# Kernel optimization log

Hardware: AMD Instinct MI355X
Metric: run time of the kernel (lower is better)

## Reference

```python
import jax, jax.numpy as jnp
import numpy as np

B, T, D, H, L = 2048, 100, 51, 128, 3  # batch, window, vars, latent, layers


def _lstm_cell(x, h, c, Wih, Whh, b):
    # PyTorch gate order: i, f, g, o. b = b_ih + b_hh (mathematically identical).
    g = x @ Wih.T + h @ Whh.T + b
    i, f, gg, o = jnp.split(g, 4, axis=-1)
    i = jax.nn.sigmoid(i)
    f = jax.nn.sigmoid(f)
    gg = jnp.tanh(gg)
    o = jax.nn.sigmoid(o)
    c_new = f * c + i * gg
    h_new = o * jnp.tanh(c_new)
    return h_new, c_new


def _run_layer(xs, Wih, Whh, b):
    # xs: [T, B, in]; returns full h sequence and final (h, c)
    bsz = xs.shape[1]
    h0 = jnp.zeros((bsz, H), xs.dtype)
    c0 = jnp.zeros((bsz, H), xs.dtype)

    def step(carry, x):
        h, c = carry
        h, c = _lstm_cell(x, h, c, Wih, Whh, b)
        return (h, c), h

    (hT, cT), hs = jax.lax.scan(step, (h0, c0), xs)
    return hs, hT, cT


def setup_inputs() -> dict:
    key = jax.random.key(0)
    ks = iter(jax.random.split(key, 32))
    s = 0.05

    def w(shape):
        return jax.random.normal(next(ks), shape, dtype=jnp.float32) * s

    inp = {"src": jax.random.normal(next(ks), (B, T, D), dtype=jnp.float32)}
    # encoder LSTM params (layer0 input=D, layers1-2 input=H)
    for l in range(L):
        din = D if l == 0 else H
        inp[f"eW{l}"] = w((4 * H, din))
        inp[f"eU{l}"] = w((4 * H, H))
        inp[f"eb{l}"] = w((4 * H,))
    # decoder LSTM params (same input sizes: input_size=input_dim)
    for l in range(L):
        din = D if l == 0 else H
        inp[f"dW{l}"] = w((4 * H, din))
        inp[f"dU{l}"] = w((4 * H, H))
        inp[f"db{l}"] = w((4 * H,))
    inp["fW"] = w((D, H))
    inp["fb"] = w((D,))
    return inp


def reference(src, eW0, eU0, eb0, eW1, eU1, eb1, eW2, eU2, eb2,
              dW0, dU0, db0, dW1, dU1, db1, dW2, dU2, db2, fW, fb):
    bsz, seq, dvar = src.shape
    xs = jnp.transpose(src, (1, 0, 2))  # [T, B, D]

    # ----- encoder: 3 stacked LSTM layers (dropout is identity at eval) -----
    enc = [(eW0, eU0, eb0), (eW1, eU1, eb1), (eW2, eU2, eb2)]
    hs_fin, cs_fin = [], []
    cur = xs
    for (Wih, Whh, b) in enc:
        cur, hT, cT = _run_layer(cur, Wih, Whh, b)
        hs_fin.append(hT)
        cs_fin.append(cT)

    dec = [(dW0, dU0, db0), (dW1, dU1, db1), (dW2, dU2, db2)]
    x0 = jnp.zeros((bsz, dvar), src.dtype)

    def dec_step(carry, _):
        x, (h0, h1, h2), (c0, c1, c2) = carry
        h0, c0 = _lstm_cell(x, h0, c0, *dec[0])
        h1, c1 = _lstm_cell(h0, h1, c1, *dec[1])
        h2, c2 = _lstm_cell(h1, h2, c2, *dec[2])
        pred = h2 @ fW.T + fb  # note: self.relu is defined but never applied
        return (pred, (h0, h1, h2), (c0, c1, c2)), pred

    carry0 = (x0, tuple(hs_fin), tuple(cs_fin))
    _, preds = jax.lax.scan(dec_step, carry0, None, length=seq)  # [T, B, D]

    # cat along time then reverse time axis (inv_idx)
    out = jnp.transpose(preds, (1, 0, 2))[:, ::-1, :]
    return out
```

## Files before the change

kernel.cpp:

```cpp
#include <hip/hip_runtime.h>
#include <stdint.h>

#define Tn 100
#define Dn 51
#define Hn 128
#define G4 512
#define BR 8
#define NWG 256
#define NTH 1024
#define RP 264

typedef unsigned int uint32;
typedef unsigned short u16;
typedef short s16x8 __attribute__((ext_vector_type(8)));
typedef float f32x4v __attribute__((ext_vector_type(4)));

__device__ __forceinline__ float rcp_(float x){ return __builtin_amdgcn_rcpf(x); }
__device__ __forceinline__ float sigm(float x){ return rcp_(1.f + __expf(-x)); }
__device__ __forceinline__ float tanh_(float x){ return 1.f - 2.f*rcp_(1.f + __expf(2.f*x)); }

__device__ __forceinline__ u16 f2bf(float f){
  uint32 u = __float_as_uint(f);
  return (u16)((u + 0x7fffu + ((u >> 16) & 1u)) >> 16);
}
__device__ __forceinline__ float bf2f(u16 u){ return __uint_as_float(((uint32)u)<<16); }

__device__ __forceinline__ void wr_xh(u16* __restrict__ xhA, int r, int k, float v){
  u16 h = f2bf(v);
  xhA[r*RP + k]     = h;
  xhA[(r+8)*RP + k] = f2bf(v - bf2f(h));
}

struct WP {
  const float* W[6];
  const float* U[6];
  const float* Bb[6];
  const float* fW;
  const float* fb;
};

#define PREP_TOTAL (6*131072 + 6*512 + 8192 + 64)
__global__ void prep_kernel(WP p, u16* __restrict__ wsw, float* __restrict__ bias,
                            float* __restrict__ fwt, float* __restrict__ fbw)
{
  int gid = blockIdx.x*256 + threadIdx.x;
  if (gid >= PREP_TOTAL) return;
  if (gid < 6*131072){
    int l = gid >> 17;
    int e = gid & 131071;
    int n    = e >> 12;
    int s    = (e >> 9) & 7;
    int lane = (e >> 3) & 63;
    int j    = e & 7;
    int k = s*32 + (lane >> 4)*8 + j;
    int c = n*16 + (lane & 15);
    int din = (l % 3 == 0) ? Dn : Hn;
    int K = din + Hn;
    u16 v = 0;
    if (k < K){
      float f = (k < din) ? p.W[l][(size_t)c*din + k] : p.U[l][(size_t)c*Hn + (k - din)];
      v = f2bf(f);
    }
    wsw[gid] = v;
  } else if (gid < 6*131072 + 6*512){
    int i = gid - 6*131072;
    bias[i] = p.Bb[i>>9][i & 511];
  } else if (gid < 6*131072 + 6*512 + 8192){
    int i = gid - (6*131072 + 6*512);
    int k = i >> 6, d = i & 63;
    fwt[i] = (d < Dn) ? p.fW[(size_t)d*Hn + k] : 0.f;
  } else {
    int d = gid - (6*131072 + 6*512 + 8192);
    fbw[d] = (d < Dn) ? p.fb[d] : 0.f;
  }
}

template<int S>
__device__ __forceinline__ void gemm_mfma(const u16* __restrict__ wsl,
                                          const float* __restrict__ bl,
                                          const u16* __restrict__ xhA,
                                          float* __restrict__ gates, int tid)
{
  const int wave = tid >> 6, lane = tid & 63;
  const int mrow = lane & 15, kgrp = lane >> 4;
  const int n0 = wave*2;
  const u16* bp0 = wsl + n0*4096 + lane*8;
  const int aoff = mrow*RP + kgrp*8;
  f32x4v acc0 = {0.f,0.f,0.f,0.f}, acc1 = {0.f,0.f,0.f,0.f};
  #pragma unroll 2
  for (int s=0; s<S; s++){
    s16x8 a  = *(const s16x8*)(xhA + aoff + s*32);
    s16x8 b0 = *(const s16x8*)(bp0 + s*512);
    s16x8 b1 = *(const s16x8*)(bp0 + 4096 + s*512);
    acc0 = __builtin_amdgcn_mfma_f32_16x16x32_bf16(a, b0, acc0, 0, 0, 0);
    acc1 = __builtin_amdgcn_mfma_f32_16x16x32_bf16(a, b1, acc1, 0, 0, 0);
  }
  #pragma unroll
  for (int v=0; v<4; v++){
    float l0 = __shfl_down(acc0[v], 32);
    float l1 = __shfl_down(acc1[v], 32);
    acc0[v] += l0;
    acc1[v] += l1;
  }
  if (kgrp < 2){
    int rb = kgrp*4;
    int c0g = n0*16 + mrow, c1g = c0g + 16;
    float bv0 = bl[c0g], bv1 = bl[c1g];
    #pragma unroll
    for (int v=0; v<4; v++){
      gates[(rb+v)*G4 + c0g] = acc0[v] + bv0;
      gates[(rb+v)*G4 + c1g] = acc1[v] + bv1;
    }
  }
}

__device__ __forceinline__ void activate(const float* __restrict__ gates,
                                         float* __restrict__ h, float* __restrict__ c, int tid)
{
  int r = tid >> 7, j = tid & 127;
  const float* g = gates + r*G4;
  float ig = sigm (g[j]);
  float fg = sigm (g[j + Hn]);
  float gg = tanh_(g[j + 2*Hn]);
  float og = sigm (g[j + 3*Hn]);
  int hi = r*Hn + j;
  float cn = fg*c[hi] + ig*gg;
  c[hi] = cn;
  h[hi] = og*tanh_(cn);
}

__device__ __forceinline__ void build_src(u16* __restrict__ xhA,
                                          const float* __restrict__ src,
                                          long b0, int t, const float* __restrict__ h0, int tid)
{
  int k = tid & 255;
  #pragma unroll
  for (int it=0; it<2; it++){
    int r = (tid >> 8) + it*4;
    if (k < 192){
      float v;
      if (k < Dn) v = src[((size_t)(b0+r)*Tn + t)*Dn + k];
      else if (k < Dn + Hn) v = h0[r*Hn + (k - Dn)];
      else v = 0.f;
      wr_xh(xhA, r, k, v);
    }
  }
}

__device__ __forceinline__ void build_pred(u16* __restrict__ xhA,
                                           const float* __restrict__ pred,
                                           const float* __restrict__ h0, int tid)
{
  int k = tid & 255;
  #pragma unroll
  for (int it=0; it<2; it++){
    int r = (tid >> 8) + it*4;
    if (k < 192){
      float v;
      if (k < Dn) v = pred[r*64 + k];
      else if (k < Dn + Hn) v = h0[r*Hn + (k - Dn)];
      else v = 0.f;
      wr_xh(xhA, r, k, v);
    }
  }
}

__device__ __forceinline__ void build_mid(u16* __restrict__ xhA,
                                          const float* __restrict__ hlow,
                                          const float* __restrict__ hl, int tid)
{
  int k = tid & 255;
  #pragma unroll
  for (int it=0; it<2; it++){
    int r = (tid >> 8) + it*4;
    float v = (k < Hn) ? hlow[r*Hn + k] : hl[r*Hn + (k - Hn)];
    wr_xh(xhA, r, k, v);
  }
}

__device__ __forceinline__ void proj_out(const float* __restrict__ h2, const float* __restrict__ fwt,
                                         const float* __restrict__ fbw, float* __restrict__ pred,
                                         float* __restrict__ out, long b0, int t, int tid)
{
  if (tid < 512){
    int r = tid >> 6, d = tid & 63;
    const float* h = h2 + r*Hn;
    float acc = 0.f;
    #pragma unroll 8
    for (int k=0;k<Hn;k++) acc += h[k] * fwt[k*64 + d];
    if (d < Dn){
      float pv = acc + fbw[d];
      pred[r*64 + d] = pv;
      out[((size_t)(b0+r)*Tn + (Tn-1-t))*Dn + d] = pv;
    }
  }
}

__global__ __launch_bounds__(NTH, 4) void lstm_kernel(
    const float* __restrict__ src, const u16* __restrict__ wsw,
    const float* __restrict__ bias, const float* __restrict__ fwt,
    const float* __restrict__ fbw, float* __restrict__ out)
{
  __shared__ __align__(16) u16   xhA[16*RP];
  __shared__ __align__(16) float gates[BR*G4];
  __shared__ __align__(16) float hS[3*BR*Hn];
  __shared__ __align__(16) float cS[3*BR*Hn];
  __shared__ __align__(16) float pred[BR*64];

  const int tid = threadIdx.x;
  const long b0 = (long)blockIdx.x * BR;

  for (int i=tid; i<16*RP; i+=NTH) xhA[i]=0;
  for (int i=tid; i<3*BR*Hn; i+=NTH){ hS[i]=0.f; cS[i]=0.f; }
  __syncthreads();

  for (int t=0;t<Tn;t++){
    build_src(xhA, src, b0, t, hS, tid);
    __syncthreads();
    gemm_mfma<6>(wsw + 0*131072, bias + 0*G4, xhA, gates, tid);
    __syncthreads();
    activate(gates, hS, cS, tid);
    __syncthreads();

    build_mid(xhA, hS, hS + BR*Hn, tid);
    __syncthreads();
    gemm_mfma<8>(wsw + 1*131072, bias + 1*G4, xhA, gates, tid);
    __syncthreads();
    activate(gates, hS + BR*Hn, cS + BR*Hn, tid);
    __syncthreads();

    build_mid(xhA, hS + BR*Hn, hS + 2*BR*Hn, tid);
    __syncthreads();
    gemm_mfma<8>(wsw + 2*131072, bias + 2*G4, xhA, gates, tid);
    __syncthreads();
    activate(gates, hS + 2*BR*Hn, cS + 2*BR*Hn, tid);
    __syncthreads();
  }

  if (tid < 512) pred[tid] = 0.f;
  __syncthreads();

  for (int t=0;t<Tn;t++){
    build_pred(xhA, pred, hS, tid);
    __syncthreads();
    gemm_mfma<6>(wsw + 3*131072, bias + 3*G4, xhA, gates, tid);
    __syncthreads();
    activate(gates, hS, cS, tid);
    __syncthreads();

    build_mid(xhA, hS, hS + BR*Hn, tid);
    __syncthreads();
    gemm_mfma<8>(wsw + 4*131072, bias + 4*G4, xhA, gates, tid);
    __syncthreads();
    activate(gates, hS + BR*Hn, cS + BR*Hn, tid);
    __syncthreads();

    build_mid(xhA, hS + BR*Hn, hS + 2*BR*Hn, tid);
    __syncthreads();
    gemm_mfma<8>(wsw + 5*131072, bias + 5*G4, xhA, gates, tid);
    __syncthreads();
    activate(gates, hS + 2*BR*Hn, cS + 2*BR*Hn, tid);
    __syncthreads();

    proj_out(hS + 2*BR*Hn, fwt, fbw, pred, out, b0, t, tid);
    __syncthreads();
  }
}

extern "C" void kernel_launch(void* const* d_in, const int* in_sizes, int n_in,
                              void* d_out, int out_size, void* d_ws, size_t ws_size,
                              hipStream_t stream)
{
  (void)in_sizes; (void)n_in; (void)out_size; (void)ws_size;
  const float* src = (const float*)d_in[0];
  WP p;
  for (int l=0;l<3;l++){
    p.W[l]    = (const float*)d_in[1  + 3*l];
    p.U[l]    = (const float*)d_in[2  + 3*l];
    p.Bb[l]   = (const float*)d_in[3  + 3*l];
    p.W[3+l]  = (const float*)d_in[10 + 3*l];
    p.U[3+l]  = (const float*)d_in[11 + 3*l];
    p.Bb[3+l] = (const float*)d_in[12 + 3*l];
  }
  p.fW = (const float*)d_in[19];
  p.fb = (const float*)d_in[20];

  u16*   wsw  = (u16*)d_ws;
  float* bias = (float*)((char*)d_ws + 6*131072*sizeof(u16));
  float* fwt  = bias + 6*512;
  float* fbw  = fwt + 8192;

  prep_kernel<<<(PREP_TOTAL + 255)/256, 256, 0, stream>>>(p, wsw, bias, fwt, fbw);
  lstm_kernel<<<NWG, NTH, 0, stream>>>(src, wsw, bias, fwt, fbw, (float*)d_out);
}
```

Before: 2.054 ms.

## Prefetch next-layer weight fragments into registers and fuse xh building into activation

Weight B-fragments for the next layer's GEMM are loaded into registers while the current GEMM runs, so global weight loads overlap the MFMA work. Activation writes h directly into per-layer bf16 xh buffers, which removes the separate build phases and their barriers. Bias, projection weights and fc bias are staged in LDS, and src for the next step is prefetched into registers. Barriers become a lightweight waitcnt plus s_barrier. The changes add register pressure (16 vector fragments) and more LDS use, which may reduce occupancy under the 4-blocks launch bound.

```diff
diff --git a/kernel.cpp b/kernel.cpp
--- a/kernel.cpp
+++ b/kernel.cpp
@@ -75,25 +75,47 @@
   }
 }
 
+__device__ __forceinline__ void bar_lds(){
+  asm volatile("s_waitcnt lgkmcnt(0)" ::: "memory");
+  __builtin_amdgcn_s_barrier();
+  asm volatile("" ::: "memory");
+}
+
 template<int S>
-__device__ __forceinline__ void gemm_mfma(const u16* __restrict__ wsl,
-                                          const float* __restrict__ bl,
-                                          const u16* __restrict__ xhA,
+__device__ __forceinline__ void ld_frags(const u16* __restrict__ wsl, s16x8* bf, int tid){
+  const int wave = tid >> 6, lane = tid & 63;
+  const u16* bp = wsl + wave*2*4096 + lane*8;
+  #pragma unroll
+  for (int s=0; s<S; s++){
+    bf[2*s]   = *(const s16x8*)(bp + s*512);
+    bf[2*s+1] = *(const s16x8*)(bp + 4096 + s*512);
+  }
+}
+
+template<int S, int SN>
+__device__ __forceinline__ void gemm_step(s16x8* bf, const u16* __restrict__ wsn,
+                                          const float* __restrict__ blS,
+                                          const u16* __restrict__ xh,
                                           float* __restrict__ gates, int tid)
 {
   const int wave = tid >> 6, lane = tid & 63;
   const int mrow = lane & 15, kgrp = lane >> 4;
   const int n0 = wave*2;
-  const u16* bp0 = wsl + n0*4096 + lane*8;
+  const u16* np = wsn + n0*4096 + lane*8;
   const int aoff = mrow*RP + kgrp*8;
   f32x4v acc0 = {0.f,0.f,0.f,0.f}, acc1 = {0.f,0.f,0.f,0.f};
-  #pragma unroll 2
-  for (int s=0; s<S; s++){
-    s16x8 a  = *(const s16x8*)(xhA + aoff + s*32);
-    s16x8 b0 = *(const s16x8*)(bp0 + s*512);
-    s16x8 b1 = *(const s16x8*)(bp0 + 4096 + s*512);
-    acc0 = __builtin_amdgcn_mfma_f32_16x16x32_bf16(a, b0, acc0, 0, 0, 0);
-    acc1 = __builtin_amdgcn_mfma_f32_16x16x32_bf16(a, b1, acc1, 0, 0, 0);
+  constexpr int SM = (S > SN) ? S : SN;
+  #pragma unroll
+  for (int s=0; s<SM; s++){
+    if (s < S){
+      s16x8 a = *(const s16x8*)(xh + aoff + s*32);
+      acc0 = __builtin_amdgcn_mfma_f32_16x16x32_bf16(a, bf[2*s],   acc0, 0, 0, 0);
+      acc1 = __builtin_amdgcn_mfma_f32_16x16x32_bf16(a, bf[2*s+1], acc1, 0, 0, 0);
+    }
+    if (s < SN){
+      bf[2*s]   = *(const s16x8*)(np + s*512);
+      bf[2*s+1] = *(const s16x8*)(np + 4096 + s*512);
+    }
   }
   #pragma unroll
   for (int v=0; v<4; v++){
@@ -105,7 +127,7 @@
   if (kgrp < 2){
     int rb = kgrp*4;
     int c0g = n0*16 + mrow, c1g = c0g + 16;
-    float bv0 = bl[c0g], bv1 = bl[c1g];
+    float bv0 = blS[c0g], bv1 = blS[c1g];
     #pragma unroll
     for (int v=0; v<4; v++){
       gates[(rb+v)*G4 + c0g] = acc0[v] + bv0;
@@ -114,8 +136,10 @@
   }
 }
 
-__device__ __forceinline__ void activate(const float* __restrict__ gates,
-                                         float* __restrict__ h, float* __restrict__ c, int tid)
+__device__ __forceinline__ void activate2(const float* __restrict__ gates,
+                                          float* __restrict__ h, float* __restrict__ c,
+                                          u16* __restrict__ xh_self, int din_self,
+                                          u16* __restrict__ xh_next, int tid)
 {
   int r = tid >> 7, j = tid & 127;
   const float* g = gates + r*G4;
@@ -126,60 +150,36 @@
   int hi = r*Hn + j;
   float cn = fg*c[hi] + ig*gg;
   c[hi] = cn;
-  h[hi] = og*tanh_(cn);
-}
-
-__device__ __forceinline__ void build_src(u16* __restrict__ xhA,
-                                          const float* __restrict__ src,
-                                          long b0, int t, const float* __restrict__ h0, int tid)
+  float hv = og*tanh_(cn);
+  h[hi] = hv;
+  wr_xh(xh_self, r, din_self + j, hv);
+  if (xh_next) wr_xh(xh_next, r, j, hv);
+}
+
+__device__ __forceinline__ void ld_src(const float* __restrict__ src, long b0, int t,
+                                       int tid, float& sA, float& sB)
 {
   int k = tid & 255;
-  #pragma unroll
-  for (int it=0; it<2; it++){
-    int r = (tid >> 8) + it*4;
-    if (k < 192){
-      float v;
-      if (k < Dn) v = src[((size_t)(b0+r)*Tn + t)*Dn + k];
-      else if (k < Dn + Hn) v = h0[r*Hn + (k - Dn)];
-      else v = 0.f;
-      wr_xh(xhA, r, k, v);
-    }
-  }
-}
-
-__device__ __forceinline__ void build_pred(u16* __restrict__ xhA,
-                                           const float* __restrict__ pred,
-                                           const float* __restrict__ h0, int tid)
+  if (k < Dn){
+    int r0 = tid >> 8;
+    sA = src[((size_t)(b0+r0)*Tn + t)*Dn + k];
+    sB = src[((size_t)(b0+r0+4)*Tn + t)*Dn + k];
+  }
+}
+__device__ __forceinline__ void st_src(u16* __restrict__ xh0, int tid, float sA, float sB)
 {
   int k = tid & 255;
-  #pragma unroll
-  for (int it=0; it<2; it++){
-    int r = (tid >> 8) + it*4;
-    if (k < 192){
-      float v;
-      if (k < Dn) v = pred[r*64 + k];
-      else if (k < Dn + Hn) v = h0[r*Hn + (k - Dn)];
-      else v = 0.f;
-      wr_xh(xhA, r, k, v);
-    }
-  }
-}
-
-__device__ __forceinline__ void build_mid(u16* __restrict__ xhA,
-                                          const float* __restrict__ hlow,
-                                          const float* __restrict__ hl, int tid)
-{
-  int k = tid & 255;
-  #pragma unroll
-  for (int it=0; it<2; it++){
-    int r = (tid >> 8) + it*4;
-    float v = (k < Hn) ? hlow[r*Hn + k] : hl[r*Hn + (k - Hn)];
-    wr_xh(xhA, r, k, v);
-  }
-}
-
-__device__ __forceinline__ void proj_out(const float* __restrict__ h2, const float* __restrict__ fwt,
-                                         const float* __restrict__ fbw, float* __restrict__ pred,
+  if (k < Dn){
+    int r0 = tid >> 8;
+    wr_xh(xh0, r0,   k, sA);
+    wr_xh(xh0, r0+4, k, sB);
+  }
+}
+
+__device__ __forceinline__ void proj_out(const float* __restrict__ h2,
+                                         const float* __restrict__ fwtS,
+                                         const float* __restrict__ fbwS,
+                                         u16* __restrict__ xh0,
                                          float* __restrict__ out, long b0, int t, int tid)
 {
   if (tid < 512){
@@ -187,11 +187,11 @@
     const float* h = h2 + r*Hn;
     float acc = 0.f;
     #pragma unroll 8
-    for (int k=0;k<Hn;k++) acc += h[k] * fwt[k*64 + d];
+    for (int k=0;k<Hn;k++) acc += h[k] * fwtS[k*64 + d];
     if (d < Dn){
-      float pv = acc + fbw[d];
-      pred[r*64 + d] = pv;
+      float pv = acc + fbwS[d];
       out[((size_t)(b0+r)*Tn + (Tn-1-t))*Dn + d] = pv;
+      wr_xh(xh0, r, d, pv);
     }
   }
 }
@@ -201,69 +201,80 @@
     const float* __restrict__ bias, const float* __restrict__ fwt,
     const float* __restrict__ fbw, float* __restrict__ out)
 {
-  __shared__ __align__(16) u16   xhA[16*RP];
+  __shared__ __align__(16) u16   xhA[3*16*RP];
   __shared__ __align__(16) float gates[BR*G4];
   __shared__ __align__(16) float hS[3*BR*Hn];
   __shared__ __align__(16) float cS[3*BR*Hn];
-  __shared__ __align__(16) float pred[BR*64];
+  __shared__ __align__(16) float fwtS[8192];
+  __shared__ __align__(16) float biasS[6*G4];
+  __shared__ __align__(16) float fbwS[64];
 
   const int tid = threadIdx.x;
   const long b0 = (long)blockIdx.x * BR;
-
-  for (int i=tid; i<16*RP; i+=NTH) xhA[i]=0;
+  u16* xh0 = xhA;
+  u16* xh1 = xhA + 16*RP;
+  u16* xh2 = xhA + 32*RP;
+
+  const u16* wsE0 = wsw;
+  const u16* wsE1 = wsw + 1*131072;
+  const u16* wsE2 = wsw + 2*131072;
+  const u16* wsD0 = wsw + 3*131072;
+  const u16* wsD1 = wsw + 4*131072;
+  const u16* wsD2 = wsw + 5*131072;
+
+  s16x8 bf[16];
+  float sA = 0.f, sB = 0.f;
+
+  ld_src(src, b0, 0, tid, sA, sB);
+  for (int i=tid; i<8192; i+=NTH) fwtS[i] = fwt[i];
+  for (int i=tid; i<6*G4; i+=NTH) biasS[i] = bias[i];
+  if (tid < 64) fbwS[tid] = fbw[tid];
+  ld_frags<6>(wsE0, bf, tid);
+  for (int i=tid; i<3*16*RP; i+=NTH) xhA[i]=0;
   for (int i=tid; i<3*BR*Hn; i+=NTH){ hS[i]=0.f; cS[i]=0.f; }
-  __syncthreads();
+  bar_lds();
+  st_src(xh0, tid, sA, sB);
+  bar_lds();
 
   for (int t=0;t<Tn;t++){
-    build_src(xhA, src, b0, t, hS, tid);
-    __syncthreads();
-    gemm_mfma<6>(wsw + 0*131072, bias + 0*G4, xhA, gates, tid);
-    __syncthreads();
-    activate(gates, hS, cS, tid);
-    __syncthreads();
-
-    build_mid(xhA, hS, hS + BR*Hn, tid);
-    __syncthreads();
-    gemm_mfma<8>(wsw + 1*131072, bias + 1*G4, xhA, gates, tid);
-    __syncthreads();
-    activate(gates, hS + BR*Hn, cS + BR*Hn, tid);
-    __syncthreads();
-
-    build_mid(xhA, hS + BR*Hn, hS + 2*BR*Hn, tid);
-    __syncthreads();
-    gemm_mfma<8>(wsw + 2*131072, bias + 2*G4, xhA, gates, tid);
-    __syncthreads();
-    activate(gates, hS + 2*BR*Hn, cS + 2*BR*Hn, tid);
-    __syncthreads();
-  }
-
-  if (tid < 512) pred[tid] = 0.f;
-  __syncthreads();
+    gemm_step<6,8>(bf, wsE1, biasS + 0*G4, xh0, gates, tid);
+    bar_lds();
+    activate2(gates, hS,         cS,         xh0, Dn, xh1, tid);
+    bar_lds();
+    gemm_step<8,8>(bf, wsE2, biasS + 1*G4, xh1, gates, tid);
+    bar_lds();
+    activate2(gates, hS + BR*Hn, cS + BR*Hn, xh1, Hn, xh2, tid);
+    bar_lds();
+    int tn = (t < Tn-1) ? t+1 : Tn-1;
+    ld_src(src, b0, tn, tid, sA, sB);
+    gemm_step<8,6>(bf, (t < Tn-1) ? wsE0 : wsD0, biasS + 2*G4, xh2, gates, tid);
+    bar_lds();
+    activate2(gates, hS + 2*BR*Hn, cS + 2*BR*Hn, xh2, Hn, (u16*)nullptr, tid);
+    if (t < Tn-1) st_src(xh0, tid, sA, sB);
+    bar_lds();
+  }
+
+  {
+    int r = tid >> 7, k = tid & 127;
+    if (k < Dn){ xh0[r*RP + k] = 0; xh0[(r+8)*RP + k] = 0; }
+  }
+  bar_lds();
 
   for (int t=0;t<Tn;t++){
-    build_pred(xhA, pred, hS, tid);
-    __syncthreads();
-    gemm_mfma<6>(wsw + 3*131072, bias + 3*G4, xhA, gates, tid);
-    __syncthreads();
-    activate(gates, hS, cS, tid);
-    __syncthreads();
-
-    build_mid(xhA, hS, hS + BR*Hn, tid);
-    __syncthreads();
-    gemm_mfma<8>(wsw + 4*131072, bias + 4*G4, xhA, gates, tid);
-    __syncthreads();
-    activate(gates, hS + BR*Hn, cS + BR*Hn, tid);
-    __syncthreads();
-
-    build_mid(xhA, hS + BR*Hn, hS + 2*BR*Hn, tid);
-    __syncthreads();
-    gemm_mfma<8>(wsw + 5*131072, bias + 5*G4, xhA, gates, tid);
-    __syncthreads();
-    activate(gates, hS + 2*BR*Hn, cS + 2*BR*Hn, tid);
-    __syncthreads();
-
-    proj_out(hS + 2*BR*Hn, fwt, fbw, pred, out, b0, t, tid);
-    __syncthreads();
+    gemm_step<6,8>(bf, wsD1, biasS + 3*G4, xh0, gates, tid);
+    bar_lds();
+    activate2(gates, hS,         cS,         xh0, Dn, xh1, tid);
+    bar_lds();
+    gemm_step<8,8>(bf, wsD2, biasS + 4*G4, xh1, gates, tid);
+    bar_lds();
+    activate2(gates, hS + BR*Hn, cS + BR*Hn, xh1, Hn, xh2, tid);
+    bar_lds();
+    gemm_step<8,6>(bf, wsD0, biasS + 5*G4, xh2, gates, tid);
+    bar_lds();
+    activate2(gates, hS + 2*BR*Hn, cS + 2*BR*Hn, xh2, Hn, (u16*)nullptr, tid);
+    bar_lds();
+    proj_out(hS + 2*BR*Hn, fwtS, fbwS, xh0, out, b0, t, tid);
+    bar_lds();
   }
 }
 
```

New measurement: 3.355 ms. 1.63x slower.
